# Kernel tuning notes

Hardware: AMD Instinct MI355X
Metric: run time of the kernel (lower is better)

Reference implementation:

```python
import jax, jax.numpy as jnp
import numpy as np

# Dims: B INRs, N probe points, d_in=2 coords, hidden H, out D_OUT, proj P
B, N, D_IN, H, D_OUT, P = 128, 4096, 2, 128, 3, 128
W0_SIREN = 30.0  # SIREN frequency scale
LN_EPS = 1e-5


def setup_inputs() -> dict:
    key = jax.random.key(0)
    ks = jax.random.split(key, 12)
    sn = lambda k, shape, sc: (jax.random.normal(k, shape, dtype=jnp.float32) * sc)
    return {
        # per-sample SIREN params, torch layout: weight [b, in, out, 1], bias [b, out, 1]
        "w0": sn(ks[0], (B, D_IN, H, 1), 1.0 / D_IN),
        "w1": sn(ks[1], (B, H, H, 1), np.sqrt(6.0 / H) / W0_SIREN),
        "w2": sn(ks[2], (B, H, D_OUT, 1), np.sqrt(6.0 / H) / W0_SIREN),
        "b0": sn(ks[3], (B, H, 1), 0.1),
        "b1": sn(ks[4], (B, H, 1), 0.1),
        "b2": sn(ks[5], (B, D_OUT, 1), 0.1),
        # learned probe coordinates, initialized U[-1, 1) as in the module
        "inputs": jax.random.uniform(ks[6], (1, N, D_IN), dtype=jnp.float32, minval=-1.0, maxval=1.0),
        # projection (num_inputs -> proj_dim) + LayerNorm params, one per probed layer (4 total)
        "pw": sn(ks[7], (4, N, P), 1.0 / np.sqrt(N)),
        "pb": jnp.zeros((4, P), jnp.float32),
        "ln_g": jnp.ones((4, P), jnp.float32),
        "ln_b": jnp.zeros((4, P), jnp.float32),
    }


def _layernorm(x, g, b):
    m = jnp.mean(x, axis=-1, keepdims=True)
    v = jnp.mean(jnp.square(x - m), axis=-1, keepdims=True)
    return (x - m) * jax.lax.rsqrt(v + LN_EPS) * g + b


def reference(w0, w1, w2, b0, b1, b2, inputs, pw, pb, ln_g, ln_b):
    b = w0.shape[0]
    x = jnp.broadcast_to(inputs, (b,) + inputs.shape[1:])  # [b, n, d_in]

    def lin(h, W, bb):
        # per-sample linear: [b,n,i] @ [b,i,o] + [b,1,o]
        return jnp.einsum('bni,bio->bno', h, W[..., 0]) + bb[:, None, :, 0]

    h1 = jnp.sin(W0_SIREN * lin(x, w0, b0))   # [b, n, H]
    h2 = jnp.sin(W0_SIREN * lin(h1, w1, b1))  # [b, n, H]
    h3 = lin(h2, w2, b2)                      # [b, n, D_OUT] (last layer: no sine)
    feats = [x, h1, h2, h3]  # probe features per node layer (input coords + activations)

    outs = []
    for i, f in enumerate(feats):
        # permute to [b, dim_i, n], project n -> P, then LayerNorm over P
        z = jnp.einsum('bnd,np->bdp', f, pw[i]) + pb[i]
        outs.append(_layernorm(z, ln_g[i], ln_b[i]))
    return jnp.concatenate(outs, axis=1)  # [b, d_in + H + H + D_OUT, P]
```

## Files before the change

kernel.cpp:

```cpp
#include <hip/hip_runtime.h>


typedef unsigned short u16;
typedef __attribute__((ext_vector_type(8))) short short8;
typedef __attribute__((ext_vector_type(4))) short short4v;
typedef __attribute__((ext_vector_type(4))) float f32x4;
typedef __attribute__((ext_vector_type(4))) float float4v;

#define DEV __device__ __forceinline__

DEV float b2f(u16 h){ return __uint_as_float(((unsigned)h) << 16); }
DEV u16 f2b(float f){
  unsigned u = __float_as_uint(f);
  return (u16)((u + 0x7FFFu + ((u >> 16) & 1u)) >> 16);
}
DEV float sin_fast(float x){
  float r = x * 0.15915494309189535f;
  r = r - rintf(r);
#if __has_builtin(__builtin_amdgcn_sinf)
  return __builtin_amdgcn_sinf(r);
#else
  return __sinf(r * 6.283185307179586f);
#endif
}
template<int C> DEV float dpp_add(float x){
  int yi = __builtin_amdgcn_update_dpp(0, __float_as_int(x), C, 0xF, 0xF, true);
  return x + __int_as_float(yi);
}
DEV float sum16(float x){
  x = dpp_add<0x128>(x); x = dpp_add<0x124>(x);
  x = dpp_add<0x122>(x); x = dpp_add<0x121>(x);
  return x;
}

DEV int is_bf16_fmt(const void* lng){ return *(const unsigned*)lng == 0x3F803F80u; }
struct In {
  const float* f; const u16* h; int bf;
  DEV In(const void* p, int b_) : f((const float*)p), h((const u16*)p), bf(b_) {}
  DEV float at(size_t i) const { return bf ? b2f(h[i]) : f[i]; }
};

__global__ __launch_bounds__(256) void k_prep(const void* pwv, const void* inpv,
                                              const void* lngv,
                                              u16* __restrict__ pwT,
                                              float* __restrict__ xbuf){
  const int bf = is_bf16_fmt(lngv);
  const int t = threadIdx.x;
  if (blockIdx.x == 256){
    In inp(inpv, bf);
    for (int i = t; i < 8192; i += 256) xbuf[i] = inp.at(i);
    return;
  }
  In pw(pwv, bf);
  __shared__ u16 tile[64 * 129];
  const int layer = blockIdx.x >> 6;
  const int n0 = (blockIdx.x & 63) * 64;
  const size_t base = ((size_t)layer * 4096 + n0) * 128;
#pragma unroll
  for (int k = 0; k < 32; k++){
    int idx = k * 256 + t, n = idx >> 7, p = idx & 127;
    tile[n * 129 + p] = f2b(pw.at(base + (size_t)n * 128 + p));
  }
  __syncthreads();
  u16* dst = pwT + (size_t)layer * 128 * 4096 + n0;
#pragma unroll
  for (int k = 0; k < 32; k++){
    int idx = k * 256 + t, p = idx >> 6, n = idx & 63;
    dst[(size_t)p * 4096 + n] = tile[n * 129 + p];
  }
}

#define S_NK 136
#define S_T  40

template<bool PARTIAL>
__global__ __launch_bounds__(512, 2)
void k_main(const void* w0v, const void* w1v, const void* w2v,
            const void* b0v, const void* b1v, const void* b2v,
            const void* pbv, const void* lgv, const void* lbv,
            const u16* __restrict__ pwTg, const float* __restrict__ xbuf,
            float* __restrict__ outp, int TS){
  __shared__ __align__(16) u16 spw[4][128 * S_T];
  __shared__ __align__(16) u16 sh1nk[32 * S_NK];
  __shared__ __align__(16) u16 sh1T[128 * S_T];
  __shared__ __align__(16) u16 sh2T[128 * S_T];
  __shared__ __align__(16) u16 sxT[16 * S_T];
  __shared__ float sW2[512];
  __shared__ float sb2[4];
  __shared__ float sPB[512], sG[512], sBB[512];

  float* sP1 = (float*)sh1nk;
  float* sP2 = (float*)sh1T;
  float* sM  = (float*)sh2T;
  float* sI  = (float*)sh2T + 512;

  const int bf = is_bf16_fmt(lgv);
  In w0(w0v, bf), w1(w1v, bf), w2(w2v, bf), b0(b0v, bf), b1(b1v, bf),
     b2(b2v, bf), pb(pbv, bf), lg(lgv, bf), lb(lbv, bf);

  const int t = threadIdx.x;
  const int b = blockIdx.x & 127, sseg = blockIdx.x >> 7;
  const int lane = t & 63, wave = t >> 6, quad = lane >> 4, r16 = lane & 15;
  const int oo = wave * 16 + r16;

  if (t >= 256 && t < 384){
    int i = t - 256;
    sW2[i * 4 + 0] = w2.at(((size_t)b * 128 + i) * 3 + 0);
    sW2[i * 4 + 1] = w2.at(((size_t)b * 128 + i) * 3 + 1);
    sW2[i * 4 + 2] = w2.at(((size_t)b * 128 + i) * 3 + 2);
    sW2[i * 4 + 3] = 0.f;
  }
  if (t < 4) sb2[t] = (t < 3) ? b2.at(b * 3 + t) : 0.f;
  sPB[t] = pb.at(t); sG[t] = lg.at(t); sBB[t] = lb.at(t);
  for (int k = t; k < 16 * S_T; k += 512) sxT[k] = 0;

  const int p1n = t >> 4, p1hb = (t & 15) * 8;
  float w00[8], w01[8], b00[8];
#pragma unroll
  for (int j = 0; j < 8; j++){
    w00[j] = w0.at((size_t)b * 256 + p1hb + j);
    w01[j] = w0.at((size_t)b * 256 + 128 + p1hb + j);
    b00[j] = b0.at((size_t)b * 128 + p1hb + j);
  }
  const int p2h = t & 127, p2nb = (t >> 7) * 8;
  const float q00 = w0.at((size_t)b * 256 + p2h);
  const float q01 = w0.at((size_t)b * 256 + 128 + p2h);
  const float qb0 = b0.at((size_t)b * 128 + p2h);
  const float bias1 = b1.at((size_t)b * 128 + oo);

  short8 w1f[4];
#pragma unroll
  for (int ks = 0; ks < 4; ks++){
#pragma unroll
    for (int j = 0; j < 8; j++)
      w1f[ks][j] = (short)f2b(w1.at((size_t)b * 16384 +
                                    (size_t)(ks * 32 + quad * 8 + j) * 128 + oo));
  }
  short8 a1s = {0,0,0,0,0,0,0,0};
  if (r16 == 0){
#pragma unroll
    for (int j = 0; j < 8; j++) a1s[j] = (short)0x3F80;
  }

  const int pwrow = t >> 2, pwc = t & 3;
  const u16* pwsrc = pwTg + (size_t)pwrow * 4096 + pwc * 8;
  const int pwdofs = pwrow * S_T + pwc * 8;
  const int bofs = oo * S_T + quad * 8;

  const f32x4 zz = {0.f,0.f,0.f,0.f};
  f32x4 az1[8], az2[8], ay[8], az0 = zz, az3 = zz;
#pragma unroll
  for (int i = 0; i < 8; i++){ az1[i] = zz; az2[i] = zz; ay[i] = zz; }

  const int n0first = sseg * TS * 32;
  short8 pwv[4];
#pragma unroll
  for (int L = 0; L < 4; L++)
    pwv[L] = *(const short8*)(pwsrc + (size_t)L * 524288 + n0first);
  float2 xp1 = *(const float2*)(xbuf + (size_t)(n0first + p1n) * 2);

  __syncthreads();

  for (int nt = 0; nt < TS; nt++){
    const int n0 = (sseg * TS + nt) * 32;

    float4v xq[4];
#pragma unroll
    for (int q = 0; q < 4; q++)
      xq[q] = *(const float4v*)(xbuf + (size_t)(n0 + p2nb) * 2 + q * 4);
#pragma unroll
    for (int L = 0; L < 4; L++)
      *(short8*)&spw[L][pwdofs] = pwv[L];
    if ((t & 15) == 0){
      sxT[p1n] = f2b(xp1.x);
      sxT[S_T + p1n] = f2b(xp1.y);
    }
    {
      short8 v;
#pragma unroll
      for (int j = 0; j < 8; j++)
        v[j] = (short)f2b(sin_fast(30.f * fmaf(xp1.y, w01[j], fmaf(xp1.x, w00[j], b00[j]))));
      *(short8*)&sh1nk[p1n * S_NK + p1hb] = v;
    }
    {
      short8 v;
#pragma unroll
      for (int j = 0; j < 8; j++){
        float x0 = xq[j >> 1][(j & 1) * 2], x1 = xq[j >> 1][(j & 1) * 2 + 1];
        v[j] = (short)f2b(sin_fast(30.f * fmaf(x1, q01, fmaf(x0, q00, qb0))));
      }
      *(short8*)&sh1T[p2h * S_T + p2nb] = v;
    }
    __syncthreads();

    {
      const int nn = (nt + 1 < TS) ? nt + 1 : nt;
      const int n0n = (sseg * TS + nn) * 32;
      short8 pwn[4];
#pragma unroll
      for (int L = 0; L < 4; L++)
        pwn[L] = *(const short8*)(pwsrc + (size_t)L * 524288 + n0n);
      float2 xp1n = *(const float2*)(xbuf + (size_t)(n0n + p1n) * 2);

      f32x4 h0 = zz, h1a = zz;
#pragma unroll
      for (int ks = 0; ks < 4; ks++){
        h0  = __builtin_amdgcn_mfma_f32_16x16x32_bf16(
                *(short8*)&sh1nk[r16 * S_NK + ks * 32 + quad * 8], w1f[ks], h0, 0, 0, 0);
        h1a = __builtin_amdgcn_mfma_f32_16x16x32_bf16(
                *(short8*)&sh1nk[(16 + r16) * S_NK + ks * 32 + quad * 8], w1f[ks], h1a, 0, 0, 0);
      }
      az0 = __builtin_amdgcn_mfma_f32_16x16x32_bf16(
              *(short8*)&sxT[r16 * S_T + quad * 8], *(short8*)&spw[0][bofs], az0, 0, 0, 0);
#pragma unroll
      for (int mb = 0; mb < 8; mb++)
        az1[mb] = __builtin_amdgcn_mfma_f32_16x16x32_bf16(
                    *(short8*)&sh1T[(mb * 16 + r16) * S_T + quad * 8],
                    *(short8*)&spw[1][bofs], az1[mb], 0, 0, 0);
      az3 = __builtin_amdgcn_mfma_f32_16x16x32_bf16(a1s, *(short8*)&spw[3][bofs], az3, 0, 0, 0);
      {
        short4v v;
#pragma unroll
        for (int r = 0; r < 4; r++) v[r] = (short)f2b(sin_fast(30.f * (h0[r] + bias1)));
        *(short4v*)&sh2T[oo * S_T + quad * 4] = v;
#pragma unroll
        for (int r = 0; r < 4; r++) v[r] = (short)f2b(sin_fast(30.f * (h1a[r] + bias1)));
        *(short4v*)&sh2T[oo * S_T + 16 + quad * 4] = v;
      }
      __syncthreads();

#pragma unroll
      for (int mb = 0; mb < 8; mb++){
        short8 a = *(short8*)&sh2T[(mb * 16 + r16) * S_T + quad * 8];
        az2[mb] = __builtin_amdgcn_mfma_f32_16x16x32_bf16(a, *(short8*)&spw[2][bofs], az2[mb], 0, 0, 0);
        ay[mb]  = __builtin_amdgcn_mfma_f32_16x16x32_bf16(a, *(short8*)&spw[3][bofs], ay[mb], 0, 0, 0);
      }

#pragma unroll
      for (int L = 0; L < 4; L++) pwv[L] = pwn[L];
      xp1 = xp1n;
    }
    __syncthreads();
  }

  const int p = oo;
  float S3 = (quad == 0) ? az3[0] : 0.f;
  S3 += __shfl_xor(S3, 16, 64); S3 += __shfl_xor(S3, 32, 64);
  float z3v[3];
#pragma unroll
  for (int d = 0; d < 3; d++){
    float a = 0.f;
#pragma unroll
    for (int mb = 0; mb < 8; mb++)
#pragma unroll
      for (int r = 0; r < 4; r++)
        a = fmaf(sW2[(mb * 16 + quad * 4 + r) * 4 + d], ay[mb][r], a);
    a += __shfl_xor(a, 16, 64); a += __shfl_xor(a, 32, 64);
    z3v[d] = a + sb2[d] * S3;
  }

  if (PARTIAL){
    float* zp = outp + ((size_t)(sseg * 128 + b)) * 261 * 128;
    if (quad == 0){
#pragma unroll
      for (int r = 0; r < 2; r++) zp[(size_t)r * 128 + p] = az0[r];
#pragma unroll
      for (int d = 0; d < 3; d++) zp[(size_t)(258 + d) * 128 + p] = z3v[d];
    }
#pragma unroll
    for (int mb = 0; mb < 8; mb++)
#pragma unroll
      for (int r = 0; r < 4; r++){
        int drow = mb * 16 + quad * 4 + r;
        zp[(size_t)(2 + drow) * 128 + p]   = az1[mb][r];
        zp[(size_t)(130 + drow) * 128 + p] = az2[mb][r];
      }
    return;
  }

  const float pb0v = sPB[p],       pb1v = sPB[128 + p];
  const float pb2v = sPB[256 + p], pb3v = sPB[384 + p];

  auto rowsum = [&](float v, int row, bool wr){
    float s1 = sum16(v), s2 = sum16(v * v);
    if (wr && r16 == 0){ sP1[row * 8 + wave] = s1; sP2[row * 8 + wave] = s2; }
  };
#pragma unroll
  for (int r = 0; r < 2; r++) rowsum(az0[r] + pb0v, r, quad == 0);
#pragma unroll
  for (int mb = 0; mb < 8; mb++)
#pragma unroll
    for (int r = 0; r < 4; r++)
      rowsum(az1[mb][r] + pb1v, 2 + mb * 16 + quad * 4 + r, true);
#pragma unroll
  for (int mb = 0; mb < 8; mb++)
#pragma unroll
    for (int r = 0; r < 4; r++)
      rowsum(az2[mb][r] + pb2v, 130 + mb * 16 + quad * 4 + r, true);
#pragma unroll
  for (int d = 0; d < 3; d++) rowsum(z3v[d] + pb3v, 258 + d, quad == 0);
  __syncthreads();

  if (t < 261){
    float s1 = 0.f, s2 = 0.f;
#pragma unroll
    for (int w = 0; w < 8; w++){ s1 += sP1[t * 8 + w]; s2 += sP2[t * 8 + w]; }
    float m = s1 * (1.f / 128.f);
    float var = fmaf(-m, m, s2 * (1.f / 128.f));
    sM[t] = m;
    sI[t] = rsqrtf(fmaxf(var, 0.f) + 1e-5f);
  }
  __syncthreads();

  const size_t ob = (size_t)b * 261 * 128;
  auto emit = [&](float v, int row, int grp){
    outp[ob + (size_t)row * 128 + p] =
      (v - sM[row]) * sI[row] * sG[grp * 128 + p] + sBB[grp * 128 + p];
  };
  if (quad == 0){
#pragma unroll
    for (int r = 0; r < 2; r++) emit(az0[r] + pb0v, r, 0);
#pragma unroll
    for (int d = 0; d < 3; d++) emit(z3v[d] + pb3v, 258 + d, 3);
  }
#pragma unroll
  for (int mb = 0; mb < 8; mb++)
#pragma unroll
    for (int r = 0; r < 4; r++)
      emit(az1[mb][r] + pb1v, 2 + mb * 16 + quad * 4 + r, 1);
#pragma unroll
  for (int mb = 0; mb < 8; mb++)
#pragma unroll
    for (int r = 0; r < 4; r++)
      emit(az2[mb][r] + pb2v, 130 + mb * 16 + quad * 4 + r, 2);
}

__global__ __launch_bounds__(256)
void k_ln(const float* __restrict__ zp, const void* pbv, const void* lgv,
          const void* lbv, float* __restrict__ out, int split){
  const int bf = is_bf16_fmt(lgv);
  In pb(pbv, bf), lg(lgv, bf), lb(lbv, bf);
  const int lane = threadIdx.x & 63;
  const int row = blockIdx.x * 4 + (threadIdx.x >> 6);
  const int b = row / 261, d = row % 261;
  const int grp = (d < 2) ? 0 : (d < 130) ? 1 : (d < 258) ? 2 : 3;
  const int p0 = lane * 2;
  float v0 = pb.at(grp * 128 + p0), v1 = pb.at(grp * 128 + p0 + 1);
  for (int s2 = 0; s2 < split; s2++){
    const float* zr = zp + ((size_t)(s2 * 128 + b) * 261 + d) * 128;
    v0 += zr[p0]; v1 += zr[p0 + 1];
  }
  float s1 = v0 + v1, s2s = v0 * v0 + v1 * v1;
#pragma unroll
  for (int o = 1; o < 64; o <<= 1){
    s1 += __shfl_xor(s1, o, 64);
    s2s += __shfl_xor(s2s, o, 64);
  }
  float m = s1 * (1.f / 128.f);
  float var = fmaf(-m, m, s2s * (1.f / 128.f));
  float inv = rsqrtf(fmaxf(var, 0.f) + 1e-5f);
  float2 o2;
  o2.x = (v0 - m) * inv * lg.at(grp * 128 + p0)     + lb.at(grp * 128 + p0);
  o2.y = (v1 - m) * inv * lg.at(grp * 128 + p0 + 1) + lb.at(grp * 128 + p0 + 1);
  *(float2*)(out + (size_t)row * 128 + p0) = o2;
}

extern "C" void kernel_launch(void* const* d_in, const int* in_sizes, int n_in,
                              void* d_out, int out_size, void* d_ws, size_t ws_size,
                              hipStream_t stream){
  const void* w0  = d_in[0];
  const void* w1  = d_in[1];
  const void* w2  = d_in[2];
  const void* b0  = d_in[3];
  const void* b1  = d_in[4];
  const void* b2  = d_in[5];
  const void* inp = d_in[6];
  const void* pw  = d_in[7];
  const void* pb  = d_in[8];
  const void* lng = d_in[9];
  const void* lnb = d_in[10];
  float* out = (float*)d_out;

  u16* pwT    = (u16*)d_ws;
  float* xbuf = (float*)((char*)d_ws + (size_t)4 * 128 * 4096 * 2);
  const size_t zoff = (size_t)4 * 128 * 4096 * 2 + 8192 * 4;
  float* zp = (float*)((char*)d_ws + zoff);
  const size_t seg = (size_t)128 * 261 * 128 * 4;

  const int split = (ws_size >= zoff + 2 * seg) ? 2 : 1;

  k_prep<<<257, 256, 0, stream>>>(pw, inp, lng, pwT, xbuf);
  if (split == 2){
    k_main<true><<<256, 512, 0, stream>>>(w0, w1, w2, b0, b1, b2,
        pb, lng, lnb, pwT, xbuf, zp, 64);
    k_ln<<<(128 * 261) / 4, 256, 0, stream>>>(zp, pb, lng, lnb, out, 2);
  } else {
    k_main<false><<<128, 512, 0, stream>>>(w0, w1, w2, b0, b1, b2,
        pb, lng, lnb, pwT, xbuf, out, 128);
  }
}
```

Before: 251.9 us.

## Software-pipeline first-layer sine computation across tiles and hoist LDS B-fragments

Computes the layer-1 sine activations for the next point tile while the current tile's MFMAs run, so the ALU-heavy sine work can overlap matrix instructions instead of sitting between barriers. It also loads the projection-weight B fragments from shared memory once per tile into registers rather than re-reading them for every MFMA. This raises register pressure through the extra live short8 vectors, which may reduce occupancy.

```diff
diff --git a/kernel.cpp b/kernel.cpp
--- a/kernel.cpp
+++ b/kernel.cpp
@@ -158,16 +158,20 @@
   for (int L = 0; L < 4; L++)
     pwv[L] = *(const short8*)(pwsrc + (size_t)L * 524288 + n0first);
   float2 xp1 = *(const float2*)(xbuf + (size_t)(n0first + p1n) * 2);
+  short8 v1, v2;
+#pragma unroll
+  for (int j = 0; j < 8; j++)
+    v1[j] = (short)f2b(sin_fast(30.f * fmaf(xp1.y, w01[j], fmaf(xp1.x, w00[j], b00[j]))));
+#pragma unroll
+  for (int q = 0; q < 4; q++){
+    float4v xa = *(const float4v*)(xbuf + (size_t)(n0first + p2nb) * 2 + q * 4);
+    v2[2 * q]     = (short)f2b(sin_fast(30.f * fmaf(xa[1], q01, fmaf(xa[0], q00, qb0))));
+    v2[2 * q + 1] = (short)f2b(sin_fast(30.f * fmaf(xa[3], q01, fmaf(xa[2], q00, qb0))));
+  }
 
   __syncthreads();
 
   for (int nt = 0; nt < TS; nt++){
-    const int n0 = (sseg * TS + nt) * 32;
-
-    float4v xq[4];
-#pragma unroll
-    for (int q = 0; q < 4; q++)
-      xq[q] = *(const float4v*)(xbuf + (size_t)(n0 + p2nb) * 2 + q * 4);
 #pragma unroll
     for (int L = 0; L < 4; L++)
       *(short8*)&spw[L][pwdofs] = pwv[L];
@@ -175,22 +179,8 @@
       sxT[p1n] = f2b(xp1.x);
       sxT[S_T + p1n] = f2b(xp1.y);
     }
-    {
-      short8 v;
-#pragma unroll
-      for (int j = 0; j < 8; j++)
-        v[j] = (short)f2b(sin_fast(30.f * fmaf(xp1.y, w01[j], fmaf(xp1.x, w00[j], b00[j]))));
-      *(short8*)&sh1nk[p1n * S_NK + p1hb] = v;
-    }
-    {
-      short8 v;
-#pragma unroll
-      for (int j = 0; j < 8; j++){
-        float x0 = xq[j >> 1][(j & 1) * 2], x1 = xq[j >> 1][(j & 1) * 2 + 1];
-        v[j] = (short)f2b(sin_fast(30.f * fmaf(x1, q01, fmaf(x0, q00, qb0))));
-      }
-      *(short8*)&sh1T[p2h * S_T + p2nb] = v;
-    }
+    *(short8*)&sh1nk[p1n * S_NK + p1hb] = v1;
+    *(short8*)&sh1T[p2h * S_T + p2nb] = v2;
     __syncthreads();
 
     {
@@ -202,6 +192,9 @@
         pwn[L] = *(const short8*)(pwsrc + (size_t)L * 524288 + n0n);
       float2 xp1n = *(const float2*)(xbuf + (size_t)(n0n + p1n) * 2);
 
+      short8 bB0 = *(short8*)&spw[0][bofs];
+      short8 bB1 = *(short8*)&spw[1][bofs];
+      short8 bB3 = *(short8*)&spw[3][bofs];
       f32x4 h0 = zz, h1a = zz;
 #pragma unroll
       for (int ks = 0; ks < 4; ks++){
@@ -211,13 +204,25 @@
                 *(short8*)&sh1nk[(16 + r16) * S_NK + ks * 32 + quad * 8], w1f[ks], h1a, 0, 0, 0);
       }
       az0 = __builtin_amdgcn_mfma_f32_16x16x32_bf16(
-              *(short8*)&sxT[r16 * S_T + quad * 8], *(short8*)&spw[0][bofs], az0, 0, 0, 0);
+              *(short8*)&sxT[r16 * S_T + quad * 8], bB0, az0, 0, 0, 0);
 #pragma unroll
       for (int mb = 0; mb < 8; mb++)
         az1[mb] = __builtin_amdgcn_mfma_f32_16x16x32_bf16(
                     *(short8*)&sh1T[(mb * 16 + r16) * S_T + quad * 8],
-                    *(short8*)&spw[1][bofs], az1[mb], 0, 0, 0);
-      az3 = __builtin_amdgcn_mfma_f32_16x16x32_bf16(a1s, *(short8*)&spw[3][bofs], az3, 0, 0, 0);
+                    bB1, az1[mb], 0, 0, 0);
+      az3 = __builtin_amdgcn_mfma_f32_16x16x32_bf16(a1s, bB3, az3, 0, 0, 0);
+
+      short8 v1n, v2n;
+#pragma unroll
+      for (int j = 0; j < 8; j++)
+        v1n[j] = (short)f2b(sin_fast(30.f * fmaf(xp1n.y, w01[j], fmaf(xp1n.x, w00[j], b00[j]))));
+#pragma unroll
+      for (int q = 0; q < 4; q++){
+        float4v xa = *(const float4v*)(xbuf + (size_t)(n0n + p2nb) * 2 + q * 4);
+        v2n[2 * q]     = (short)f2b(sin_fast(30.f * fmaf(xa[1], q01, fmaf(xa[0], q00, qb0))));
+        v2n[2 * q + 1] = (short)f2b(sin_fast(30.f * fmaf(xa[3], q01, fmaf(xa[2], q00, qb0))));
+      }
+
       {
         short4v v;
 #pragma unroll
@@ -229,16 +234,17 @@
       }
       __syncthreads();
 
+      short8 bB2 = *(short8*)&spw[2][bofs];
 #pragma unroll
       for (int mb = 0; mb < 8; mb++){
         short8 a = *(short8*)&sh2T[(mb * 16 + r16) * S_T + quad * 8];
-        az2[mb] = __builtin_amdgcn_mfma_f32_16x16x32_bf16(a, *(short8*)&spw[2][bofs], az2[mb], 0, 0, 0);
-        ay[mb]  = __builtin_amdgcn_mfma_f32_16x16x32_bf16(a, *(short8*)&spw[3][bofs], ay[mb], 0, 0, 0);
+        az2[mb] = __builtin_amdgcn_mfma_f32_16x16x32_bf16(a, bB2, az2[mb], 0, 0, 0);
+        ay[mb]  = __builtin_amdgcn_mfma_f32_16x16x32_bf16(a, bB3, ay[mb], 0, 0, 0);
       }
 
 #pragma unroll
       for (int L = 0; L < 4; L++) pwv[L] = pwn[L];
-      xp1 = xp1n;
+      xp1 = xp1n; v1 = v1n; v2 = v2n;
     }
     __syncthreads();
   }
```

Result: slower. 260.5 us (+3.4%).

## Double-buffer h2 and pw2/pw3 tiles to defer layer-2 projection and drop a barrier

Applied to the files above, without the earlier changes.

Double-buffers the h2 activation tile and the projection weight tiles for layers 2 and 3 in shared memory. The h2 projection MFMAs for each tile now run one iteration later, overlapping the next tile's h1 sine compute, and a drain step after the loop handles the last tile. This removes one __syncthreads per iteration. The cost is extra LDS (about 30 KB more), which could hurt occupancy at 2 blocks of 512 threads per CU.

```diff
diff --git a/kernel.cpp b/kernel.cpp
--- a/kernel.cpp
+++ b/kernel.cpp
@@ -80,10 +80,11 @@
             const void* pbv, const void* lgv, const void* lbv,
             const u16* __restrict__ pwTg, const float* __restrict__ xbuf,
             float* __restrict__ outp, int TS){
-  __shared__ __align__(16) u16 spw[4][128 * S_T];
+  __shared__ __align__(16) u16 spw01[2][128 * S_T];
+  __shared__ __align__(16) u16 spw23[2][2][128 * S_T];
   __shared__ __align__(16) u16 sh1nk[32 * S_NK];
   __shared__ __align__(16) u16 sh1T[128 * S_T];
-  __shared__ __align__(16) u16 sh2T[128 * S_T];
+  __shared__ __align__(16) u16 sh2T[2][128 * S_T];
   __shared__ __align__(16) u16 sxT[16 * S_T];
   __shared__ float sW2[512];
   __shared__ float sb2[4];
@@ -161,6 +162,7 @@
 
   __syncthreads();
 
+  int cb = 0;
   for (int nt = 0; nt < TS; nt++){
     const int n0 = (sseg * TS + nt) * 32;
 
@@ -168,9 +170,10 @@
 #pragma unroll
     for (int q = 0; q < 4; q++)
       xq[q] = *(const float4v*)(xbuf + (size_t)(n0 + p2nb) * 2 + q * 4);
-#pragma unroll
-    for (int L = 0; L < 4; L++)
-      *(short8*)&spw[L][pwdofs] = pwv[L];
+    *(short8*)&spw01[0][pwdofs] = pwv[0];
+    *(short8*)&spw01[1][pwdofs] = pwv[1];
+    *(short8*)&spw23[cb][0][pwdofs] = pwv[2];
+    *(short8*)&spw23[cb][1][pwdofs] = pwv[3];
     if ((t & 15) == 0){
       sxT[p1n] = f2b(xp1.x);
       sxT[S_T + p1n] = f2b(xp1.y);
@@ -190,6 +193,17 @@
         v[j] = (short)f2b(sin_fast(30.f * fmaf(x1, q01, fmaf(x0, q00, qb0))));
       }
       *(short8*)&sh1T[p2h * S_T + p2nb] = v;
+    }
+    if (nt){
+      const u16* s2p  = sh2T[cb ^ 1];
+      const short8 bb2 = *(const short8*)&spw23[cb ^ 1][0][bofs];
+      const short8 bb3 = *(const short8*)&spw23[cb ^ 1][1][bofs];
+#pragma unroll
+      for (int mb = 0; mb < 8; mb++){
+        short8 a = *(const short8*)&s2p[(mb * 16 + r16) * S_T + quad * 8];
+        az2[mb] = __builtin_amdgcn_mfma_f32_16x16x32_bf16(a, bb2, az2[mb], 0, 0, 0);
+        ay[mb]  = __builtin_amdgcn_mfma_f32_16x16x32_bf16(a, bb3, ay[mb], 0, 0, 0);
+      }
     }
     __syncthreads();
 
@@ -211,29 +225,21 @@
                 *(short8*)&sh1nk[(16 + r16) * S_NK + ks * 32 + quad * 8], w1f[ks], h1a, 0, 0, 0);
       }
       az0 = __builtin_amdgcn_mfma_f32_16x16x32_bf16(
-              *(short8*)&sxT[r16 * S_T + quad * 8], *(short8*)&spw[0][bofs], az0, 0, 0, 0);
+              *(short8*)&sxT[r16 * S_T + quad * 8], *(short8*)&spw01[0][bofs], az0, 0, 0, 0);
 #pragma unroll
       for (int mb = 0; mb < 8; mb++)
         az1[mb] = __builtin_amdgcn_mfma_f32_16x16x32_bf16(
                     *(short8*)&sh1T[(mb * 16 + r16) * S_T + quad * 8],
-                    *(short8*)&spw[1][bofs], az1[mb], 0, 0, 0);
-      az3 = __builtin_amdgcn_mfma_f32_16x16x32_bf16(a1s, *(short8*)&spw[3][bofs], az3, 0, 0, 0);
+                    *(short8*)&spw01[1][bofs], az1[mb], 0, 0, 0);
+      az3 = __builtin_amdgcn_mfma_f32_16x16x32_bf16(a1s, *(short8*)&spw23[cb][1][bofs], az3, 0, 0, 0);
       {
         short4v v;
 #pragma unroll
         for (int r = 0; r < 4; r++) v[r] = (short)f2b(sin_fast(30.f * (h0[r] + bias1)));
-        *(short4v*)&sh2T[oo * S_T + quad * 4] = v;
+        *(short4v*)&sh2T[cb][oo * S_T + quad * 4] = v;
 #pragma unroll
         for (int r = 0; r < 4; r++) v[r] = (short)f2b(sin_fast(30.f * (h1a[r] + bias1)));
-        *(short4v*)&sh2T[oo * S_T + 16 + quad * 4] = v;
-      }
-      __syncthreads();
-
-#pragma unroll
-      for (int mb = 0; mb < 8; mb++){
-        short8 a = *(short8*)&sh2T[(mb * 16 + r16) * S_T + quad * 8];
-        az2[mb] = __builtin_amdgcn_mfma_f32_16x16x32_bf16(a, *(short8*)&spw[2][bofs], az2[mb], 0, 0, 0);
-        ay[mb]  = __builtin_amdgcn_mfma_f32_16x16x32_bf16(a, *(short8*)&spw[3][bofs], ay[mb], 0, 0, 0);
+        *(short4v*)&sh2T[cb][oo * S_T + 16 + quad * 4] = v;
       }
 
 #pragma unroll
@@ -241,6 +247,19 @@
       xp1 = xp1n;
     }
     __syncthreads();
+    cb ^= 1;
+  }
+
+  {
+    const u16* s2p  = sh2T[cb ^ 1];
+    const short8 bb2 = *(const short8*)&spw23[cb ^ 1][0][bofs];
+    const short8 bb3 = *(const short8*)&spw23[cb ^ 1][1][bofs];
+#pragma unroll
+    for (int mb = 0; mb < 8; mb++){
+      short8 a = *(const short8*)&s2p[(mb * 16 + r16) * S_T + quad * 8];
+      az2[mb] = __builtin_amdgcn_mfma_f32_16x16x32_bf16(a, bb2, az2[mb], 0, 0, 0);
+      ay[mb]  = __builtin_amdgcn_mfma_f32_16x16x32_bf16(a, bb3, ay[mb], 0, 0, 0);
+    }
   }
 
   const int p = oo;
```

Result: faster. 245.6 us (-2.5%).
